# Kernel tuning notes

Measured on AMD Instinct MI355X. Metric: run time of the kernel, lower is better.

Reference implementation:

```python
import jax, jax.numpy as jnp
import numpy as np


def setup_inputs() -> dict:
    key = jax.random.key(0)
    kx, kw = jax.random.split(key)
    B, D, H, W, K = 32, 128, 64, 64, 1024
    x = jax.random.normal(kx, (B, D, H, W), dtype=jnp.float32)
    # matches torch init: uniform(-1/k, 1/k), shape (d, k)
    weight = jax.random.uniform(kw, (D, K), dtype=jnp.float32,
                                minval=-1.0 / K, maxval=1.0 / K)
    return {"x": x, "weight": weight}


def reference(x, weight):
    # x: [B, d, H, W], weight (codebook emb): [d, k]
    # argmin of L2 norm == argmin of squared distance:
    x2 = jnp.sum(x * x, axis=1)                      # [B, H, W]
    e2 = jnp.sum(weight * weight, axis=0)            # [k]
    xe = jnp.einsum('bdhw,dk->bhwk', x, weight)      # [B, H, W, k]
    d2 = x2[..., None] - 2.0 * xe + e2               # [B, H, W, k]
    argmin = jnp.argmin(d2, axis=-1)                 # [B, H, W] int
    # gather codebook rows then move channel dim back to axis 1
    result = jnp.take(weight.T, argmin, axis=0)      # [B, H, W, d]
    result = jnp.transpose(result, (0, 3, 1, 2))     # [B, d, H, W]
    return result, argmin
```

## Files before the change

### kernel.cpp

```cpp
#include <hip/hip_runtime.h>
#include <math.h>

#define DD   128
#define KK   1024
#define HWW  4096
#define NPIX 131072
#define EPS  1.5e-4f
#define CAPA 32768
#define CAPB 8192

#define WS_WT    0
#define WS_E2    131072
#define WS_CTR   132096
#define WS_LISTA 132160
#define WS_LISTB 230464
#define WS_BHI   246848
#define WS_BLO   312384

typedef short  short8  __attribute__((ext_vector_type(8)));
typedef float  floatx4 __attribute__((ext_vector_type(4)));

static __device__ __forceinline__ unsigned short f2bf(float x) {
    unsigned u = __float_as_uint(x);
    return (unsigned short)((u + 0x7fffu + ((u >> 16) & 1u)) >> 16);
}
static __device__ __forceinline__ float bf2f(unsigned short b) {
    return __uint_as_float(((unsigned)b) << 16);
}

__global__ __launch_bounds__(256) void prep_all(
        const float* __restrict__ w,
        float* __restrict__ wT, float* __restrict__ e2,
        short8* __restrict__ bhi, short8* __restrict__ blo,
        int* __restrict__ ctr) {
    int t = blockIdx.x * 256 + threadIdx.x;
    if (t < 32768) {
        int k = t & 1023, d4 = t >> 10;
        float4 v;
        v.x = w[(d4 * 4 + 0) * KK + k];
        v.y = w[(d4 * 4 + 1) * KK + k];
        v.z = w[(d4 * 4 + 2) * KK + k];
        v.w = w[(d4 * 4 + 3) * KK + k];
        *(float4*)(wT + (size_t)k * DD + d4 * 4) = v;
    } else if (t < 49152) {
        int u     = t - 32768;
        int lane  = u & 63;
        int chunk = (u >> 6) & 3;
        int ktile = u >> 8;
        int kcol  = ktile * 16 + (lane & 15);
        int d0    = chunk * 32 + (lane >> 4) * 8;
        short8 h, l;
#pragma unroll
        for (int j = 0; j < 8; ++j) {
            float wv = w[(size_t)(d0 + j) * KK + kcol];
            unsigned short hb = f2bf(wv);
            h[j] = (short)hb;
            l[j] = (short)f2bf(wv - bf2f(hb));
        }
        bhi[u] = h;
        blo[u] = l;
    } else if (t < 50176) {
        int k = t - 49152;
        if (k == 0) { ctr[0] = 0; ctr[1] = 0; }
        float acc = 0.0f;
        for (int d = 0; d < DD; ++d) {
            float v = w[d * KK + k];
            acc = __fadd_rn(acc, __fmul_rn(v, v));
        }
        e2[k] = acc;
    }
}

__global__ __launch_bounds__(256) void vq_screen(
        const float* __restrict__ x,
        const float* __restrict__ wT,
        const float* __restrict__ e2,
        const short8* __restrict__ bhi,
        const short8* __restrict__ blo,
        float* __restrict__ out,
        int* __restrict__ listA,
        int* __restrict__ listB,
        int* __restrict__ ctr) {
    __shared__ int sk1[4][32];

    const int tid  = threadIdx.x;
    const int wave = tid >> 6;
    const int lane = tid & 63;
    const int q    = lane >> 4;
    const int col  = lane & 15;

    const int b       = blockIdx.x >> 5;
    const int base_hw = (blockIdx.x & 31) * 128 + wave * 32;

    short8 a0h[4], a0l[4], a1h[4], a1l[4];
#pragma unroll
    for (int c = 0; c < 4; ++c) {
#pragma unroll
        for (int j = 0; j < 8; ++j) {
            int d = c * 32 + q * 8 + j;
            const float* xr = x + (size_t)(b * DD + d) * HWW + base_hw;
            float x0 = xr[col];
            float x1 = xr[16 + col];
            unsigned short h0 = f2bf(x0), h1 = f2bf(x1);
            a0h[c][j] = (short)h0;  a0l[c][j] = (short)f2bf(x0 - bf2f(h0));
            a1h[c][j] = (short)h1;  a1l[c][j] = (short)f2bf(x1 - bf2f(h1));
        }
    }

    float s1[8], s2[8], s3[8];
    int   c1[8], c2[8];
#pragma unroll
    for (int i = 0; i < 8; ++i) {
        s1[i] = INFINITY; s2[i] = INFINITY; s3[i] = INFINITY;
        c1[i] = 0; c2[i] = 0;
    }

    const short8* pbh = bhi + lane;
    const short8* pbl = blo + lane;
    short8 nh0 = pbh[0],   nh1 = pbh[64],  nh2 = pbh[128], nh3 = pbh[192];
    short8 nl0 = pbl[0],   nl1 = pbl[64],  nl2 = pbl[128], nl3 = pbl[192];

    for (int kt = 0; kt < KK / 16; ++kt) {
        short8 bh0 = nh0, bh1 = nh1, bh2 = nh2, bh3 = nh3;
        short8 bl0 = nl0, bl1 = nl1, bl2 = nl2, bl3 = nl3;
        const int nb = ((kt + 1) & 63) * 256;
        nh0 = pbh[nb];  nh1 = pbh[nb + 64];  nh2 = pbh[nb + 128];  nh3 = pbh[nb + 192];
        nl0 = pbl[nb];  nl1 = pbl[nb + 64];  nl2 = pbl[nb + 128];  nl3 = pbl[nb + 192];
        float e2v = e2[kt * 16 + col];

        floatx4 p00 = {0.f,0.f,0.f,0.f}, p01 = {0.f,0.f,0.f,0.f};
        floatx4 p10 = {0.f,0.f,0.f,0.f}, p11 = {0.f,0.f,0.f,0.f};
        p00 = __builtin_amdgcn_mfma_f32_16x16x32_bf16(a0h[0], bh0, p00, 0,0,0);
        p01 = __builtin_amdgcn_mfma_f32_16x16x32_bf16(a0h[1], bh1, p01, 0,0,0);
        p00 = __builtin_amdgcn_mfma_f32_16x16x32_bf16(a0h[2], bh2, p00, 0,0,0);
        p01 = __builtin_amdgcn_mfma_f32_16x16x32_bf16(a0h[3], bh3, p01, 0,0,0);
        p00 = __builtin_amdgcn_mfma_f32_16x16x32_bf16(a0h[0], bl0, p00, 0,0,0);
        p01 = __builtin_amdgcn_mfma_f32_16x16x32_bf16(a0h[1], bl1, p01, 0,0,0);
        p00 = __builtin_amdgcn_mfma_f32_16x16x32_bf16(a0h[2], bl2, p00, 0,0,0);
        p01 = __builtin_amdgcn_mfma_f32_16x16x32_bf16(a0h[3], bl3, p01, 0,0,0);
        p00 = __builtin_amdgcn_mfma_f32_16x16x32_bf16(a0l[0], bh0, p00, 0,0,0);
        p01 = __builtin_amdgcn_mfma_f32_16x16x32_bf16(a0l[1], bh1, p01, 0,0,0);
        p00 = __builtin_amdgcn_mfma_f32_16x16x32_bf16(a0l[2], bh2, p00, 0,0,0);
        p01 = __builtin_amdgcn_mfma_f32_16x16x32_bf16(a0l[3], bh3, p01, 0,0,0);
        p10 = __builtin_amdgcn_mfma_f32_16x16x32_bf16(a1h[0], bh0, p10, 0,0,0);
        p11 = __builtin_amdgcn_mfma_f32_16x16x32_bf16(a1h[1], bh1, p11, 0,0,0);
        p10 = __builtin_amdgcn_mfma_f32_16x16x32_bf16(a1h[2], bh2, p10, 0,0,0);
        p11 = __builtin_amdgcn_mfma_f32_16x16x32_bf16(a1h[3], bh3, p11, 0,0,0);
        p10 = __builtin_amdgcn_mfma_f32_16x16x32_bf16(a1h[0], bl0, p10, 0,0,0);
        p11 = __builtin_amdgcn_mfma_f32_16x16x32_bf16(a1h[1], bl1, p11, 0,0,0);
        p10 = __builtin_amdgcn_mfma_f32_16x16x32_bf16(a1h[2], bl2, p10, 0,0,0);
        p11 = __builtin_amdgcn_mfma_f32_16x16x32_bf16(a1h[3], bl3, p11, 0,0,0);
        p10 = __builtin_amdgcn_mfma_f32_16x16x32_bf16(a1l[0], bh0, p10, 0,0,0);
        p11 = __builtin_amdgcn_mfma_f32_16x16x32_bf16(a1l[1], bh1, p11, 0,0,0);
        p10 = __builtin_amdgcn_mfma_f32_16x16x32_bf16(a1l[2], bh2, p10, 0,0,0);
        p11 = __builtin_amdgcn_mfma_f32_16x16x32_bf16(a1l[3], bh3, p11, 0,0,0);

        const int kcur = kt * 16 + col;
#pragma unroll
        for (int g = 0; g < 2; ++g) {
#pragma unroll
            for (int r = 0; r < 4; ++r) {
                const int i = g * 4 + r;
                float s = fmaf(-2.0f,
                               (g == 0 ? p00[r] + p01[r] : p10[r] + p11[r]),
                               e2v);
                bool lt1 = s < s1[i];
                bool lt2 = s < s2[i];
                s3[i] = fminf(s3[i], fmaxf(s, s2[i]));
                s2[i] = fminf(s2[i], fmaxf(s, s1[i]));
                c2[i] = lt1 ? c1[i] : (lt2 ? kcur : c2[i]);
                s1[i] = fminf(s, s1[i]);
                c1[i] = lt1 ? kcur : c1[i];
            }
        }
    }

#pragma unroll
    for (int off = 1; off < 16; off <<= 1) {
#pragma unroll
        for (int i = 0; i < 8; ++i) {
            float o1 = __shfl_xor(s1[i], off);
            float o2 = __shfl_xor(s2[i], off);
            float o3 = __shfl_xor(s3[i], off);
            int   ok1 = __shfl_xor(c1[i], off);
            int   ok2 = __shfl_xor(c2[i], off);
            bool afirst = (s1[i] < o1) || (s1[i] == o1 && c1[i] < ok1);
            float n1, n2, n3; int nk1, nk2;
            if (afirst) {
                bool asec = (s2[i] < o1) || (s2[i] == o1 && c2[i] < ok1);
                n1 = s1[i]; nk1 = c1[i];
                n2 = asec ? s2[i] : o1;  nk2 = asec ? c2[i] : ok1;
                n3 = asec ? fminf(s3[i], o1) : fminf(s2[i], o2);
            } else {
                bool bsec = (o2 < s1[i]) || (o2 == s1[i] && ok2 < c1[i]);
                n1 = o1; nk1 = ok1;
                n2 = bsec ? o2 : s1[i];  nk2 = bsec ? ok2 : c1[i];
                n3 = bsec ? fminf(o3, s1[i]) : fminf(o2, s2[i]);
            }
            s1[i] = n1; s2[i] = n2; s3[i] = n3; c1[i] = nk1; c2[i] = nk2;
        }
    }

#pragma unroll
    for (int g = 0; g < 2; ++g) {
#pragma unroll
        for (int r = 0; r < 4; ++r) {
            if (col == r) {
                const int i = g * 4 + r;
                int plocal = g * 16 + q * 4 + r;
                int hwp    = base_hw + plocal;
                int Pg     = b * HWW + hwp;
                out[(size_t)DD * NPIX + Pg] = (float)c1[i];
                sk1[wave][plocal] = c1[i];
                float g12 = s2[i] - s1[i];
                float g13 = s3[i] - s1[i];
                if (g12 <= EPS) {
                    if (g13 > EPS) {
                        int idx = atomicAdd(&ctr[0], 1);
                        if (idx < CAPA) {
                            listA[3 * idx + 0] = Pg;
                            listA[3 * idx + 1] = c1[i];
                            listA[3 * idx + 2] = c2[i];
                        }
                    } else {
                        int idx = atomicAdd(&ctr[1], 1);
                        if (idx < CAPB) listB[idx] = Pg;
                    }
                }
            }
        }
    }
    __syncthreads();

    {
        const int p_lo = lane & 15;
        const int dgrp = lane >> 4;
#pragma unroll
        for (int half = 0; half < 2; ++half) {
            const int plocal = half * 16 + p_lo;
            const int kk     = sk1[wave][plocal];
            const int hwp    = base_hw + plocal;
            const float* wrow = wT + (size_t)kk * DD;
#pragma unroll
            for (int i = 0; i < 32; ++i) {
                int d = i * 4 + dgrp;
                out[(size_t)(b * DD + d) * HWW + hwp] = wrow[d];
            }
        }
    }
}

__global__ __launch_bounds__(256) void vq_resolve(
        const float* __restrict__ x,
        const float* __restrict__ wT,
        const float* __restrict__ e2,
        const int* __restrict__ listA,
        const int* __restrict__ listB,
        const int* __restrict__ ctr,
        float* __restrict__ out) {
    const int nA = min(ctr[0], CAPA);
    const int nB = min(ctr[1], CAPB);
    const int tid  = threadIdx.x;
    const int gtid = blockIdx.x * 256 + tid;
    const int wave = gtid >> 6;
    const int lane = tid & 63;
    const int NW = (gridDim.x * 256) >> 6;
    const int NT = gridDim.x * 256;

    for (int j = wave; j < nB; j += NW) {
        const int p  = listB[j];
        const int b  = p >> 12;
        const int hw = p & (HWW - 1);
        const float* xp = x + (size_t)b * DD * HWW + hw;
        float xv[DD];
#pragma unroll 4
        for (int d = 0; d < DD; ++d) xv[d] = xp[(size_t)d * HWW];
        float x2 = 0.0f;
#pragma unroll 4
        for (int d = 0; d < DD; ++d) x2 = __fadd_rn(x2, __fmul_rn(xv[d], xv[d]));

        unsigned long long best = ~0ull;
        for (int kk = 0; kk < 16; ++kk) {
            const int k = lane * 16 + kk;
            const float* wk = wT + (size_t)k * DD;
            float a = 0.0f;
#pragma unroll 4
            for (int d = 0; d < DD; ++d)
                a = __fadd_rn(a, __fmul_rn(xv[d], wk[d]));
            float d2 = __fadd_rn(__fsub_rn(x2, 2.0f * a), e2[k]);
            unsigned long long c =
                ((unsigned long long)__float_as_uint(d2) << 32) | (unsigned)k;
            best = best < c ? best : c;
        }
#pragma unroll
        for (int off = 32; off; off >>= 1) {
            unsigned long long o = __shfl_xor(best, off);
            best = best < o ? best : o;
        }
        const int kwin = (int)(best & 0xffffffffu);
        if (lane == 0) out[(size_t)DD * NPIX + p] = (float)kwin;
        const float* wb = wT + (size_t)kwin * DD;
        float* op = out + (size_t)b * DD * HWW + hw;
        op[(size_t)lane * HWW]        = wb[lane];
        op[(size_t)(lane + 64) * HWW] = wb[lane + 64];
    }

    for (int i = blockIdx.x + tid * gridDim.x; i < nA; i += NT) {
        const int p  = listA[3 * i + 0];
        const int kA = listA[3 * i + 1];
        const int kB = listA[3 * i + 2];
        const int b  = p >> 12;
        const int hw = p & (HWW - 1);
        const float* xp = x + (size_t)b * DD * HWW + hw;
        const float* wa = wT + (size_t)kA * DD;
        const float* wb = wT + (size_t)kB * DD;
        float x2 = 0.0f, aa = 0.0f, ab = 0.0f;
#pragma unroll 4
        for (int d = 0; d < DD; ++d) {
            float xd = xp[(size_t)d * HWW];
            x2 = __fadd_rn(x2, __fmul_rn(xd, xd));
            aa = __fadd_rn(aa, __fmul_rn(xd, wa[d]));
            ab = __fadd_rn(ab, __fmul_rn(xd, wb[d]));
        }
        float dA = __fadd_rn(__fsub_rn(x2, 2.0f * aa), e2[kA]);
        float dB = __fadd_rn(__fsub_rn(x2, 2.0f * ab), e2[kB]);
        const int kwin = (dA < dB || (dA == dB && kA < kB)) ? kA : kB;
        out[(size_t)DD * NPIX + p] = (float)kwin;
        const float* ww = wT + (size_t)kwin * DD;
        float* op = out + (size_t)b * DD * HWW + hw;
#pragma unroll 8
        for (int d = 0; d < DD; ++d) op[(size_t)d * HWW] = ww[d];
    }
}

extern "C" void kernel_launch(void* const* d_in, const int* in_sizes, int n_in,
                              void* d_out, int out_size, void* d_ws, size_t ws_size,
                              hipStream_t stream) {
    const float* x = (const float*)d_in[0];
    const float* w = (const float*)d_in[1];
    float* out = (float*)d_out;
    float* wsf = (float*)d_ws;

    float*  wT    = wsf + WS_WT;
    float*  e2    = wsf + WS_E2;
    int*    ctr   = (int*)(wsf + WS_CTR);
    int*    listA = (int*)(wsf + WS_LISTA);
    int*    listB = (int*)(wsf + WS_LISTB);
    short8* bhi   = (short8*)(wsf + WS_BHI);
    short8* blo   = (short8*)(wsf + WS_BLO);

    prep_all  <<<dim3(196),  dim3(256), 0, stream>>>(w, wT, e2, bhi, blo, ctr);
    vq_screen <<<dim3(1024), dim3(256), 0, stream>>>(x, wT, e2, bhi, blo, out,
                                                     listA, listB, ctr);
    vq_resolve<<<dim3(256),  dim3(256), 0, stream>>>(x, wT, e2, listA, listB,
                                                     ctr, out);
}
```

Baseline: 452.5 us.

## Stage codebook tiles in LDS via async loads and lag top-3 update

Each block now loads the bf16 hi/lo codebook tiles once into a double-buffered LDS array using global_load_lds, shared by its four waves. Previously every wave prefetched the full tile into registers from global memory. The top-3 compare/select for a tile is also deferred by one iteration, so it overlaps with the next tile's MFMA chain. The cost is a block-wide barrier on every k-tile and extra LDS reads, which could stall waves that would otherwise run independently.

```diff
diff --git a/kernel.cpp b/kernel.cpp
--- a/kernel.cpp
+++ b/kernel.cpp
@@ -81,7 +81,8 @@
         int* __restrict__ listA,
         int* __restrict__ listB,
         int* __restrict__ ctr) {
-    __shared__ int sk1[4][32];
+    __shared__ int    sk1[4][32];
+    __shared__ short8 sB[2][2][256];
 
     const int tid  = threadIdx.x;
     const int wave = tid >> 6;
@@ -109,24 +110,62 @@
 
     float s1[8], s2[8], s3[8];
     int   c1[8], c2[8];
+    float prevS[8];
+    float prevE2 = 0.0f;
 #pragma unroll
     for (int i = 0; i < 8; ++i) {
         s1[i] = INFINITY; s2[i] = INFINITY; s3[i] = INFINITY;
         c1[i] = 0; c2[i] = 0;
-    }
-
-    const short8* pbh = bhi + lane;
-    const short8* pbl = blo + lane;
-    short8 nh0 = pbh[0],   nh1 = pbh[64],  nh2 = pbh[128], nh3 = pbh[192];
-    short8 nl0 = pbl[0],   nl1 = pbl[64],  nl2 = pbl[128], nl3 = pbl[192];
-
-    for (int kt = 0; kt < KK / 16; ++kt) {
-        short8 bh0 = nh0, bh1 = nh1, bh2 = nh2, bh3 = nh3;
-        short8 bl0 = nl0, bl1 = nl1, bl2 = nl2, bl3 = nl3;
-        const int nb = ((kt + 1) & 63) * 256;
-        nh0 = pbh[nb];  nh1 = pbh[nb + 64];  nh2 = pbh[nb + 128];  nh3 = pbh[nb + 192];
-        nl0 = pbl[nb];  nl1 = pbl[nb + 64];  nl2 = pbl[nb + 128];  nl3 = pbl[nb + 192];
-        float e2v = e2[kt * 16 + col];
+        prevS[i] = -INFINITY;
+    }
+
+    auto top3_update = [&](int ktile) {
+        const int kcur = ktile * 16 + col;
+#pragma unroll
+        for (int g = 0; g < 2; ++g) {
+#pragma unroll
+            for (int r = 0; r < 4; ++r) {
+                const int i = g * 4 + r;
+                float s = fmaf(-2.0f, prevS[i], prevE2);
+                bool lt1 = s < s1[i];
+                bool lt2 = s < s2[i];
+                s3[i] = fminf(s3[i], fmaxf(s, s2[i]));
+                s2[i] = fminf(s2[i], fmaxf(s, s1[i]));
+                c2[i] = lt1 ? c1[i] : (lt2 ? kcur : c2[i]);
+                s1[i] = fminf(s, s1[i]);
+                c1[i] = lt1 ? kcur : c1[i];
+            }
+        }
+    };
+
+    auto stage = [&](int t, int buf) {
+        const int base = t * 256 + wave * 64 + lane;
+        __builtin_amdgcn_global_load_lds((const unsigned int*)(bhi + base),
+                                         (unsigned int*)&sB[buf][0][wave * 64],
+                                         16, 0, 0);
+        __builtin_amdgcn_global_load_lds((const unsigned int*)(blo + base),
+                                         (unsigned int*)&sB[buf][1][wave * 64],
+                                         16, 0, 0);
+    };
+
+    stage(0, 0);
+    __syncthreads();
+
+    for (int kt = 0; kt < 64; ++kt) {
+        const int cur = kt & 1;
+        if (kt < 63) stage(kt + 1, cur ^ 1);
+
+        short8 bh0 = sB[cur][0][lane +   0];
+        short8 bh1 = sB[cur][0][lane +  64];
+        short8 bh2 = sB[cur][0][lane + 128];
+        short8 bh3 = sB[cur][0][lane + 192];
+        short8 bl0 = sB[cur][1][lane +   0];
+        short8 bl1 = sB[cur][1][lane +  64];
+        short8 bl2 = sB[cur][1][lane + 128];
+        short8 bl3 = sB[cur][1][lane + 192];
+        float  e2v = e2[kt * 16 + col];
+
+        top3_update(kt - 1);
 
         floatx4 p00 = {0.f,0.f,0.f,0.f}, p01 = {0.f,0.f,0.f,0.f};
         floatx4 p10 = {0.f,0.f,0.f,0.f}, p11 = {0.f,0.f,0.f,0.f};
@@ -155,25 +194,19 @@
         p10 = __builtin_amdgcn_mfma_f32_16x16x32_bf16(a1l[2], bh2, p10, 0,0,0);
         p11 = __builtin_amdgcn_mfma_f32_16x16x32_bf16(a1l[3], bh3, p11, 0,0,0);
 
-        const int kcur = kt * 16 + col;
-#pragma unroll
-        for (int g = 0; g < 2; ++g) {
-#pragma unroll
-            for (int r = 0; r < 4; ++r) {
-                const int i = g * 4 + r;
-                float s = fmaf(-2.0f,
-                               (g == 0 ? p00[r] + p01[r] : p10[r] + p11[r]),
-                               e2v);
-                bool lt1 = s < s1[i];
-                bool lt2 = s < s2[i];
-                s3[i] = fminf(s3[i], fmaxf(s, s2[i]));
-                s2[i] = fminf(s2[i], fmaxf(s, s1[i]));
-                c2[i] = lt1 ? c1[i] : (lt2 ? kcur : c2[i]);
-                s1[i] = fminf(s, s1[i]);
-                c1[i] = lt1 ? kcur : c1[i];
-            }
-        }
-    }
+        prevS[0] = p00[0] + p01[0];
+        prevS[1] = p00[1] + p01[1];
+        prevS[2] = p00[2] + p01[2];
+        prevS[3] = p00[3] + p01[3];
+        prevS[4] = p10[0] + p11[0];
+        prevS[5] = p10[1] + p11[1];
+        prevS[6] = p10[2] + p11[2];
+        prevS[7] = p10[3] + p11[3];
+        prevE2   = e2v;
+
+        __syncthreads();
+    }
+    top3_update(63);
 
 #pragma unroll
     for (int off = 1; off < 16; off <<= 1) {
```

Result: slower. 594.6 us (+31.4%).
